# Kernel optimization log

Hardware: AMD Instinct MI355X
Metric: run time of the kernel (lower is better)

Reference implementation:

```python
import jax, jax.numpy as jnp
import numpy as np

N, E, FIN, H, OUT, L = 80000, 1280000, 128, 64, 10, 3
NEG_SLOPE = 0.2


def setup_inputs() -> dict:
    key = jax.random.key(0)
    ks = jax.random.split(key, 2 + 6 * L + 2)
    inp = {
        "x": jax.random.normal(ks[0], (N, FIN), dtype=jnp.float32),
        "edge_index": jax.random.randint(ks[1], (2, E), 0, N, dtype=jnp.int32),
        "batch": jnp.zeros((N,), dtype=jnp.int32),
    }
    k = 2
    for l in range(L):
        fin = FIN if l == 0 else H
        s = 1.0 / np.sqrt(fin)
        inp[f"Wl{l}"] = jax.random.normal(ks[k + 0], (H, fin), dtype=jnp.float32) * s
        inp[f"bl{l}"] = jnp.zeros((H,), dtype=jnp.float32)
        inp[f"Wr{l}"] = jax.random.normal(ks[k + 1], (H, fin), dtype=jnp.float32) * s
        inp[f"br{l}"] = jnp.zeros((H,), dtype=jnp.float32)
        inp[f"att{l}"] = jax.random.normal(ks[k + 2], (H,), dtype=jnp.float32) * (1.0 / np.sqrt(H))
        inp[f"b{l}"] = jnp.zeros((H,), dtype=jnp.float32)
        k += 3
    inp["Wro"] = jax.random.normal(ks[k], (OUT, H), dtype=jnp.float32) * (1.0 / np.sqrt(H))
    inp["bro"] = jnp.zeros((OUT,), dtype=jnp.float32)
    return inp


def gatv2_layer(h, src, dst, Wl, bl, Wr, br, att, b):
    # PyG GATv2Conv (heads=1, share_weights=False):
    #   xl = lin_l(h) (source side), xr = lin_r(h) (target side)
    xl = h @ Wl.T + bl          # [N, H]
    xr = h @ Wr.T + br          # [N, H]
    e = jax.nn.leaky_relu(xl[src] + xr[dst], NEG_SLOPE) @ att  # [E_tot]
    # softmax over incoming edges of each destination node
    m = jax.ops.segment_max(e, dst, num_segments=N)
    ex = jnp.exp(e - m[dst])
    denom = jax.ops.segment_sum(ex, dst, num_segments=N)
    alpha = ex / denom[dst]
    out = jax.ops.segment_sum(alpha[:, None] * xl[src], dst, num_segments=N)
    return out + b


def reference(x, edge_index, batch,
              Wl0, bl0, Wr0, br0, att0, b0,
              Wl1, bl1, Wr1, br1, att1, b1,
              Wl2, bl2, Wr2, br2, att2, b2,
              Wro, bro):
    # add self-loops once (same augmented edge set used each layer)
    loop = jnp.arange(N, dtype=edge_index.dtype)
    src = jnp.concatenate([edge_index[0], loop])
    dst = jnp.concatenate([edge_index[1], loop])
    layers = [
        (Wl0, bl0, Wr0, br0, att0, b0),
        (Wl1, bl1, Wr1, br1, att1, b1),
        (Wl2, bl2, Wr2, br2, att2, b2),
    ]
    h = x
    for (Wl, bl, Wr, br, att, b) in layers:
        h = jax.nn.relu(gatv2_layer(h, src, dst, Wl, bl, Wr, br, att, b))
    # graph_level_task=False: node-level readout
    return h @ Wro.T + bro  # [N, OUT]
```

## Files before the change

### kernel.cpp

```cpp
#include <hip/hip_runtime.h>
#include <hip/hip_bf16.h>
#include <hip/hip_fp16.h>


#define NN 80000
#define EE 1280000
#define FIN 128
#define HH 64
#define OUTD 10
#define NBUK 79
#define PCH 2048
#define NCH 625

typedef __hip_bfloat16 bf16;
typedef _Float16 f16x8 __attribute__((ext_vector_type(8)));
typedef float f32x4 __attribute__((ext_vector_type(4)));

__device__ __forceinline__ float ldw(const void* p, int i, int f) {
    return f ? __bfloat162float(((const bf16*)p)[i]) : ((const float*)p)[i];
}

__global__ void detect_kernel(const unsigned* __restrict__ w, int* __restrict__ flag) {
    int lane = threadIdx.x;
    int big = 0;
    for (int i = lane; i < 2048; i += 64) {
        unsigned u = w[i];
        float a = __uint_as_float(u << 16);
        float b = __uint_as_float(u & 0xffff0000u);
        if (!(fabsf(a) <= 1024.f)) big = 1;
        if (!(fabsf(b) <= 1024.f)) big = 1;
    }
    big = (__ballot(big) != 0ull) ? 1 : 0;
    if (lane == 0) flag[0] = big ? 0 : 1;
}

__global__ void preconvert(
    const void* Wl0, const void* Wr0, const void* Wl1, const void* Wr1,
    const void* Wl2, const void* Wr2,
    const void* bl0, const void* br0, const void* bl1, const void* br1,
    const void* bl2, const void* br2,
    const void* att0, const void* att1, const void* att2,
    const void* b0, const void* b1, const void* b2,
    const void* Wro, const void* bro,
    __half* Wh0, __half* Wh1, __half* Wh2, float* small,
    const int* __restrict__ flagp)
{
    const int f = flagp[0];
    int t = blockIdx.x * 256 + threadIdx.x;
    if (t < 16384) {
        int j = t & 127, k = t >> 7;
        float v = (j < 64) ? ldw(Wl0, j * 128 + k, f) : ldw(Wr0, (j - 64) * 128 + k, f);
        Wh0[j * 128 + k] = __float2half(v);
    } else if (t < 24576) {
        int u = t - 16384; int j = u & 127, k = u >> 7;
        float v = (j < 64) ? ldw(Wl1, j * 64 + k, f) : ldw(Wr1, (j - 64) * 64 + k, f);
        Wh1[j * 64 + k] = __float2half(v);
    } else if (t < 32768) {
        int u = t - 24576; int j = u & 127, k = u >> 7;
        float v = (j < 64) ? ldw(Wl2, j * 64 + k, f) : ldw(Wr2, (j - 64) * 64 + k, f);
        Wh2[j * 64 + k] = __float2half(v);
    } else if (t < 34304) {
        int s = t - 32768;
        const void* BL[3] = { bl0, bl1, bl2 };
        const void* BR[3] = { br0, br1, br2 };
        const void* AT[3] = { att0, att1, att2 };
        const void* BB[3] = { b0, b1, b2 };
        float v = 0.f;
        if (s < 384) {
            int l = s / 128, r = s % 128;
            v = (r < 64) ? ldw(BL[l], r, f) : ldw(BR[l], r - 64, f);
        } else if (s < 576) {
            int q = s - 384; v = ldw(AT[q / 64], q % 64, f);
        } else if (s < 768) {
            int q = s - 576; v = ldw(BB[q / 64], q % 64, f);
        } else if (s < 1408) {
            v = ldw(Wro, s - 768, f);
        } else if (s < 1418) {
            v = ldw(bro, s - 1408, f);
        } else return;
        small[s] = v;
    }
}

__global__ __launch_bounds__(256) void chunkhist_kernel(const int* __restrict__ dst,
                                                        int* __restrict__ chunkcnt)
{
    __shared__ int h[NBUK];
    const int tid = threadIdx.x, c = blockIdx.x;
    for (int i = tid; i < NBUK; i += 256) h[i] = 0;
    __syncthreads();
    const int e0 = c * PCH + tid * 8;
    int4 a = *(const int4*)(dst + e0);
    int4 b = *(const int4*)(dst + e0 + 4);
    atomicAdd(&h[a.x >> 10], 1); atomicAdd(&h[a.y >> 10], 1);
    atomicAdd(&h[a.z >> 10], 1); atomicAdd(&h[a.w >> 10], 1);
    atomicAdd(&h[b.x >> 10], 1); atomicAdd(&h[b.y >> 10], 1);
    atomicAdd(&h[b.z >> 10], 1); atomicAdd(&h[b.w >> 10], 1);
    __syncthreads();
    for (int i = tid; i < NBUK; i += 256) chunkcnt[i * NCH + c] = h[i];
}

__global__ __launch_bounds__(1024) void cscan_kernel(int* __restrict__ chunkcnt,
                                                     int* __restrict__ bucket_cnt)
{
    __shared__ int s[1024];
    const int b = blockIdx.x, t = threadIdx.x;
    int v = (t < NCH) ? chunkcnt[b * NCH + t] : 0;
    s[t] = v;
    __syncthreads();
    #pragma unroll
    for (int off = 1; off < 1024; off <<= 1) {
        int u = (t >= off) ? s[t - off] : 0;
        __syncthreads();
        s[t] += u;
        __syncthreads();
    }
    if (t < NCH) chunkcnt[b * NCH + t] = s[t] - v;
    if (t == NCH - 1) bucket_cnt[b] = s[t];
}

__global__ void bscan_kernel(const int* __restrict__ bucket_cnt,
                             int* __restrict__ bucket_base)
{
    __shared__ int sc[128];
    const int t = threadIdx.x;
    sc[t] = (t < NBUK) ? bucket_cnt[t] : 0;
    __syncthreads();
    #pragma unroll
    for (int off = 1; off < 128; off <<= 1) {
        int v = (t >= off) ? sc[t - off] : 0;
        __syncthreads();
        sc[t] += v;
        __syncthreads();
    }
    if (t < NBUK) bucket_base[t] = (t == 0) ? 0 : sc[t - 1];
    if (t == 0) bucket_base[NBUK] = sc[NBUK - 1];
}

__global__ __launch_bounds__(256) void part_kernel(const int* __restrict__ src,
                                                   const int* __restrict__ dst,
                                                   const int* __restrict__ chunkcnt,
                                                   const int* __restrict__ bucket_base,
                                                   int2* __restrict__ part)
{
    __shared__ int hcnt[NBUK];
    __shared__ int sc[128];
    __shared__ int hbase[NBUK + 1];
    __shared__ int hpos[NBUK];
    __shared__ int hgb[NBUK];
    __shared__ int2 stage[PCH];
    const int tid = threadIdx.x, c = blockIdx.x;

    for (int i = tid; i < NBUK; i += 256) hcnt[i] = 0;
    __syncthreads();

    const int e0 = c * PCH + tid * 8;
    int4 sa = *(const int4*)(src + e0);
    int4 sb = *(const int4*)(src + e0 + 4);
    int4 da = *(const int4*)(dst + e0);
    int4 db = *(const int4*)(dst + e0 + 4);
    int dv[8] = { da.x, da.y, da.z, da.w, db.x, db.y, db.z, db.w };
    int sv[8] = { sa.x, sa.y, sa.z, sa.w, sb.x, sb.y, sb.z, sb.w };
    #pragma unroll
    for (int u = 0; u < 8; u++) atomicAdd(&hcnt[dv[u] >> 10], 1);
    __syncthreads();

    if (tid < 128) sc[tid] = (tid < NBUK) ? hcnt[tid] : 0;
    __syncthreads();
    #pragma unroll
    for (int off = 1; off < 128; off <<= 1) {
        int v = (tid < 128 && tid >= off) ? sc[tid - off] : 0;
        __syncthreads();
        if (tid < 128) sc[tid] += v;
        __syncthreads();
    }
    if (tid < NBUK) {
        int b = (tid == 0) ? 0 : sc[tid - 1];
        hbase[tid] = b;
        hpos[tid] = b;
        hgb[tid] = bucket_base[tid] + chunkcnt[tid * NCH + c];
    }
    if (tid == 0) hbase[NBUK] = PCH;
    __syncthreads();

    #pragma unroll
    for (int u = 0; u < 8; u++) {
        int p = atomicAdd(&hpos[dv[u] >> 10], 1);
        stage[p] = make_int2(sv[u], dv[u]);
    }
    __syncthreads();

    for (int s = tid; s < PCH; s += 256) {
        int lo = 0, hi = NBUK;
        #pragma unroll
        for (int it = 0; it < 7; it++) {
            int mid = (lo + hi) >> 1;
            if (hbase[mid] <= s) lo = mid; else hi = mid;
        }
        part[hgb[lo] + (s - hbase[lo])] = stage[s];
    }
}

__global__ __launch_bounds__(256) void hist_part_kernel(const int2* __restrict__ part,
                                                        const int* __restrict__ bucket_base,
                                                        int* __restrict__ cnt)
{
    __shared__ int lcnt[1024];
    const int b = blockIdx.x, tid = threadIdx.x;
    const int dbase = b << 10;
    for (int i = tid; i < 1024; i += 256) lcnt[i] = 0;
    __syncthreads();
    const int eb = bucket_base[b], ee = bucket_base[b + 1];
    for (int e = eb + tid; e < ee; e += 256)
        atomicAdd(&lcnt[part[e].y - dbase], 1);
    __syncthreads();
    const int nd = min(1024, NN - dbase);
    for (int i = tid; i < nd; i += 256) cnt[dbase + i] = lcnt[i];
}

__global__ void scan1(const int* __restrict__ cnt, int* __restrict__ rowptr,
                      int* __restrict__ bsums) {
    __shared__ int sh[256];
    int i = blockIdx.x * 256 + threadIdx.x;
    int tid = threadIdx.x;
    int c = (i < NN) ? cnt[i] : 0;
    sh[tid] = c;
    __syncthreads();
    #pragma unroll
    for (int off = 1; off < 256; off <<= 1) {
        int t = (tid >= off) ? sh[tid - off] : 0;
        __syncthreads();
        sh[tid] += t;
        __syncthreads();
    }
    if (i < NN) rowptr[i + 1] = sh[tid];
    if (tid == 255) bsums[blockIdx.x] = sh[255];
}

__global__ void scan2(int* __restrict__ bsums, int nb) {
    __shared__ int sh[512];
    int t = threadIdx.x;
    sh[t] = (t < nb) ? bsums[t] : 0;
    __syncthreads();
    #pragma unroll
    for (int off = 1; off < 512; off <<= 1) {
        int v = (t >= off) ? sh[t - off] : 0;
        __syncthreads();
        sh[t] += v;
        __syncthreads();
    }
    if (t < nb) bsums[t] = sh[t];
}

__global__ void scan3(int* __restrict__ rowptr, const int* __restrict__ bsums) {
    int i = blockIdx.x * 256 + threadIdx.x;
    if (i == 0) rowptr[0] = 0;
    int add = (blockIdx.x == 0) ? 0 : bsums[blockIdx.x - 1];
    if (i < NN) rowptr[i + 1] += add;
}

__global__ __launch_bounds__(256) void scatter2_kernel(const int2* __restrict__ part,
                                                       const int* __restrict__ bucket_base,
                                                       const int* __restrict__ rowptr,
                                                       int2* __restrict__ col2)
{
    __shared__ int lfill[1024];
    const int b = blockIdx.x, tid = threadIdx.x;
    const int dbase = b << 10;
    const int nd = min(1024, NN - dbase);
    for (int i = tid; i < nd; i += 256) lfill[i] = rowptr[dbase + i];
    __syncthreads();
    const int eb = bucket_base[b], ee = bucket_base[b + 1];
    for (int e = eb + tid; e < ee; e += 256) {
        int2 sd = part[e];
        int pos = atomicAdd(&lfill[sd.y - dbase], 1);
        col2[pos] = sd;
    }
}

#define ELX_S 72
#define EXR_S 68
template<int F, bool L0>
__global__ __launch_bounds__(256) void lin_mfma(const void* __restrict__ hin_,
                                                const __half* __restrict__ Wh,
                                                const float* __restrict__ biasLR,
                                                __half* __restrict__ xlh,
                                                float* __restrict__ xr,
                                                const int* __restrict__ flagp)
{
    __shared__ __align__(16) char lds[64 * ELX_S * 2 + 64 * EXR_S * 4];
    _Float16* xs  = (_Float16*)lds;
    _Float16* eXL = (_Float16*)lds;
    float*    eXR = (float*)(lds + 64 * ELX_S * 2);

    const int tid = threadIdx.x;
    const int nb = blockIdx.x * 64;
    constexpr int OPR = F / 8;

    if (L0 && flagp[0]) {
        const uint4* hp = (const uint4*)hin_;
        for (int c = tid; c < 64 * OPR; c += 256) {
            int row = c / OPR, oct = c % OPR;
            uint4 u = hp[((size_t)(nb + row) * F + oct * 8) >> 3];
            unsigned ww[4] = { u.x, u.y, u.z, u.w };
            _Float16 v[8];
            #pragma unroll
            for (int p = 0; p < 4; p++) {
                v[2 * p]     = (_Float16)__uint_as_float(ww[p] << 16);
                v[2 * p + 1] = (_Float16)__uint_as_float(ww[p] & 0xffff0000u);
            }
            int so = oct ^ (row & 7);
            *(f16x8*)&xs[row * F + so * 8] = *(f16x8*)v;
        }
    } else {
        const float4* hp = (const float4*)hin_;
        for (int c = tid; c < 64 * OPR; c += 256) {
            int row = c / OPR, oct = c % OPR;
            size_t base = ((size_t)(nb + row) * F + oct * 8) >> 2;
            float4 a = hp[base], b = hp[base + 1];
            _Float16 v[8] = { (_Float16)a.x, (_Float16)a.y, (_Float16)a.z, (_Float16)a.w,
                              (_Float16)b.x, (_Float16)b.y, (_Float16)b.z, (_Float16)b.w };
            int so = oct ^ (row & 7);
            *(f16x8*)&xs[row * F + so * 8] = *(f16x8*)v;
        }
    }
    __syncthreads();

    const int w = tid >> 6;
    const int lane = tid & 63;
    const int n = lane & 15;
    const int quad = lane >> 4;
    constexpr int NS = F / 32;

    f16x8 afr[NS];
    #pragma unroll
    for (int s = 0; s < NS; s++) {
        int o = (s * 4 + quad) ^ (n & 7);
        afr[s] = *(const f16x8*)&xs[(w * 16 + n) * F + o * 8];
    }
    __syncthreads();

    const _Float16* Whf = (const _Float16*)Wh;
    #pragma unroll
    for (int ct = 0; ct < 8; ct++) {
        float bv = biasLR[ct * 16 + n];
        f32x4 acc = { bv, bv, bv, bv };
        #pragma unroll
        for (int s = 0; s < NS; s++) {
            f16x8 bfr = *(const f16x8*)&Whf[(size_t)(ct * 16 + n) * F + s * 32 + quad * 8];
            acc = __builtin_amdgcn_mfma_f32_16x16x32_f16(afr[s], bfr, acc, 0, 0, 0);
        }
        int rbase = w * 16 + quad * 4;
        if (ct < 4) {
            #pragma unroll
            for (int rg = 0; rg < 4; rg++)
                eXL[(rbase + rg) * ELX_S + ct * 16 + n] = (_Float16)acc[rg];
        } else {
            #pragma unroll
            for (int rg = 0; rg < 4; rg++)
                eXR[(rbase + rg) * EXR_S + (ct - 4) * 16 + n] = acc[rg];
        }
    }
    __syncthreads();

    for (int c = tid; c < 512; c += 256) {
        int row = c >> 3, oct = c & 7;
        *(uint4*)&xlh[(size_t)(nb + row) * 64 + oct * 8] =
            *(const uint4*)&eXL[row * ELX_S + oct * 8];
    }
    for (int c = tid; c < 1024; c += 256) {
        int row = c >> 4, q4 = c & 15;
        *(float4*)&xr[(size_t)(nb + row) * 64 + q4 * 4] =
            *(const float4*)&eXR[row * EXR_S + q4 * 4];
    }
}

#define DECODE8(U, D) { \
    float2 _f0 = __half22float2(*(__half2*)&U.x); \
    float2 _f1 = __half22float2(*(__half2*)&U.y); \
    float2 _f2 = __half22float2(*(__half2*)&U.z); \
    float2 _f3 = __half22float2(*(__half2*)&U.w); \
    D[0]=_f0.x; D[1]=_f0.y; D[2]=_f1.x; D[3]=_f1.y; \
    D[4]=_f2.x; D[5]=_f2.y; D[6]=_f3.x; D[7]=_f3.y; }

__global__ __launch_bounds__(256) void agg4_kernel(const __half* __restrict__ xlh,
                                                   const float* __restrict__ xr,
                                                   const float* __restrict__ attf,
                                                   const float* __restrict__ bf,
                                                   const int* __restrict__ rowptr,
                                                   const int2* __restrict__ col2,
                                                   float* __restrict__ hout)
{
    const int lane = threadIdx.x & 63;
    const int g = lane >> 3;
    const int r = lane & 7;
    int iw = blockIdx.x * 4 + (threadIdx.x >> 6);
    if (iw >= NN) return;
    const int i = __builtin_amdgcn_readfirstlane(iw);

    float xri[8], att[8];
    {
        float4 xa = *(const float4*)(xr + (size_t)i * 64 + r * 8);
        float4 xb = *(const float4*)(xr + (size_t)i * 64 + r * 8 + 4);
        xri[0]=xa.x; xri[1]=xa.y; xri[2]=xa.z; xri[3]=xa.w;
        xri[4]=xb.x; xri[5]=xb.y; xri[6]=xb.z; xri[7]=xb.w;
        float4 aa = *(const float4*)(attf + r * 8);
        float4 ab = *(const float4*)(attf + r * 8 + 4);
        att[0]=aa.x; att[1]=aa.y; att[2]=aa.z; att[3]=aa.w;
        att[4]=ab.x; att[5]=ab.y; att[6]=ab.z; att[7]=ab.w;
    }

    uint4 srow = *(const uint4*)(xlh + (size_t)i * 64 + r * 8);
    float s[8]; DECODE8(srow, s);
    float ps = 0.f;
    #pragma unroll
    for (int k = 0; k < 8; k++) {
        float u = s[k] + xri[k];
        ps = fmaf(att[k], fmaf(0.4f, fabsf(u), 0.6f * u), ps);
    }
    ps += __shfl_xor(ps, 1, 64);
    ps += __shfl_xor(ps, 2, 64);
    ps += __shfl_xor(ps, 4, 64);
    float wself = __expf(fminf(ps, 60.f));

    float acc[8];
    float denom;
    if (g == 0) {
        #pragma unroll
        for (int k = 0; k < 8; k++) acc[k] = wself * s[k];
        denom = wself;
    } else {
        #pragma unroll
        for (int k = 0; k < 8; k++) acc[k] = 0.f;
        denom = 0.f;
    }

    const int e0 = rowptr[i], e1 = rowptr[i + 1];
    const int n = e1 - e0;
    const int eL = e1 - 1;

    for (int base = 0; base < n; base += 16) {
        const int j = e0 + base;
        int sa = col2[min(j + g, eL)].x;
        int sb = col2[min(j + 8 + g, eL)].x;
        uint4 ua = *(const uint4*)(xlh + (size_t)sa * 64 + r * 8);
        uint4 ub = *(const uint4*)(xlh + (size_t)sb * 64 + r * 8);
        float A[8], B[8];
        DECODE8(ua, A);
        DECODE8(ub, B);

        float pa = 0.f, pb = 0.f;
        #pragma unroll
        for (int k = 0; k < 8; k++) {
            float va = A[k] + xri[k];
            float vb = B[k] + xri[k];
            pa = fmaf(att[k], fmaf(0.4f, fabsf(va), 0.6f * va), pa);
            pb = fmaf(att[k], fmaf(0.4f, fabsf(vb), 0.6f * vb), pb);
        }
        pa += __shfl_xor(pa, 1, 64);  pb += __shfl_xor(pb, 1, 64);
        pa += __shfl_xor(pa, 2, 64);  pb += __shfl_xor(pb, 2, 64);
        pa += __shfl_xor(pa, 4, 64);  pb += __shfl_xor(pb, 4, 64);

        float wa = (base + g < n)     ? __expf(fminf(pa, 60.f)) : 0.f;
        float wb = (base + 8 + g < n) ? __expf(fminf(pb, 60.f)) : 0.f;

        #pragma unroll
        for (int k = 0; k < 8; k++) {
            acc[k] = fmaf(wa, A[k], acc[k]);
            acc[k] = fmaf(wb, B[k], acc[k]);
        }
        denom += wa + wb;
    }

    #pragma unroll
    for (int off = 8; off < 64; off <<= 1) {
        #pragma unroll
        for (int k = 0; k < 8; k++) acc[k] += __shfl_xor(acc[k], off, 64);
        denom += __shfl_xor(denom, off, 64);
    }

    if (g == 0) {
        float inv = 1.f / denom;
        float4 bfa = *(const float4*)(bf + r * 8);
        float4 bfb = *(const float4*)(bf + r * 8 + 4);
        float o0 = fmaxf(fmaf(acc[0], inv, bfa.x), 0.f);
        float o1 = fmaxf(fmaf(acc[1], inv, bfa.y), 0.f);
        float o2 = fmaxf(fmaf(acc[2], inv, bfa.z), 0.f);
        float o3 = fmaxf(fmaf(acc[3], inv, bfa.w), 0.f);
        float o4 = fmaxf(fmaf(acc[4], inv, bfb.x), 0.f);
        float o5 = fmaxf(fmaf(acc[5], inv, bfb.y), 0.f);
        float o6 = fmaxf(fmaf(acc[6], inv, bfb.z), 0.f);
        float o7 = fmaxf(fmaf(acc[7], inv, bfb.w), 0.f);
        float* op = hout + (size_t)i * 64 + r * 8;
        *(float4*)(op)     = make_float4(o0, o1, o2, o3);
        *(float4*)(op + 4) = make_float4(o4, o5, o6, o7);
    }
}

__global__ __launch_bounds__(256) void readout2_kernel(const float* __restrict__ h,
                                                       const float* __restrict__ WROf,
                                                       const float* __restrict__ brof,
                                                       void* __restrict__ out,
                                                       const int* __restrict__ flagp)
{
    __shared__ float wsh[640];
    __shared__ float bsh[OUTD];
    const int tid = threadIdx.x;
    for (int idx = tid; idx < 640; idx += 256) {
        int k = idx / 10, o = idx % 10;
        wsh[idx] = WROf[o * 64 + k];
    }
    if (tid < OUTD) bsh[tid] = brof[tid];
    __syncthreads();

    const int i = blockIdx.x * 256 + tid;
    if (i >= NN) return;
    const int f = flagp[0];

    float res[OUTD];
    #pragma unroll
    for (int o = 0; o < OUTD; o++) res[o] = bsh[o];

    const float4* h4 = (const float4*)(h + (size_t)i * 64);
    #pragma unroll 4
    for (int c = 0; c < 16; c++) {
        float4 hv = h4[c];
        const float* wp = &wsh[c * 40];
        #pragma unroll
        for (int o = 0; o < OUTD; o++) {
            float t = fmaf(hv.x, wp[o], fmaf(hv.y, wp[10 + o],
                      fmaf(hv.z, wp[20 + o], hv.w * wp[30 + o])));
            res[o] += t;
        }
    }

    if (f) {
        bf16* op = (bf16*)out + (size_t)i * OUTD;
        #pragma unroll
        for (int o = 0; o < OUTD; o++) op[o] = __float2bfloat16(res[o]);
    } else {
        float* op = (float*)out + (size_t)i * OUTD;
        #pragma unroll
        for (int o = 0; o < OUTD; o++) op[o] = res[o];
    }
}

extern "C" void kernel_launch(void* const* d_in, const int* in_sizes, int n_in,
                              void* d_out, int out_size, void* d_ws, size_t ws_size,
                              hipStream_t stream) {
    const void* x   = d_in[0];
    const int* ei   = (const int*)d_in[1];
    const void* Wl0 = d_in[3];  const void* bl0 = d_in[4];
    const void* Wr0 = d_in[5];  const void* br0 = d_in[6];
    const void* at0 = d_in[7];  const void* b0  = d_in[8];
    const void* Wl1 = d_in[9];  const void* bl1 = d_in[10];
    const void* Wr1 = d_in[11]; const void* br1 = d_in[12];
    const void* at1 = d_in[13]; const void* b1  = d_in[14];
    const void* Wl2 = d_in[15]; const void* bl2 = d_in[16];
    const void* Wr2 = d_in[17]; const void* br2 = d_in[18];
    const void* at2 = d_in[19]; const void* b2  = d_in[20];
    const void* Wro = d_in[21]; const void* bro = d_in[22];

    const int* srcArr = ei;
    const int* dstArr = ei + EE;

    float* wf = (float*)d_ws;
    __half* Wh0  = (__half*)wf;
    __half* Wh1  = (__half*)(wf + 16384);
    __half* Wh2  = (__half*)(wf + 24576);
    float* small = wf + 32768;
    int*   flag  = (int*)(wf + 34304);
    int*   rowptr = (int*)(wf + 34368);
    int*   bsums  = (int*)(wf + 114496);
    int*   fillc  = (int*)(wf + 115008);
    int*   bucket_cnt  = (int*)(wf + 195008);
    int*   bucket_base = (int*)(wf + 195136);
    int*   chunkcnt    = (int*)(wf + 195264);
    int2*  part   = (int2*)(wf + 244736);
    int2*  col2   = (int2*)(wf + 2804736);
    __half* xlh   = (__half*)(wf + 5364736);
    float* xr = wf + 7924736;
    float* hA = xr + (size_t)NN * 64;

    float* biasLR0 = small;        float* biasLR1 = small + 128; float* biasLR2 = small + 256;
    float* attf0 = small + 384;    float* attf1 = small + 448;   float* attf2 = small + 512;
    float* bf0   = small + 576;    float* bf1   = small + 640;   float* bf2   = small + 704;
    float* WROf  = small + 768;    float* brof  = small + 1408;

    detect_kernel<<<dim3(1), dim3(64), 0, stream>>>((const unsigned*)Wl0, flag);

    preconvert<<<dim3(134), dim3(256), 0, stream>>>(
        Wl0, Wr0, Wl1, Wr1, Wl2, Wr2, bl0, br0, bl1, br1, bl2, br2,
        at0, at1, at2, b0, b1, b2, Wro, bro, Wh0, Wh1, Wh2, small, flag);

    chunkhist_kernel<<<dim3(NCH), dim3(256), 0, stream>>>(dstArr, chunkcnt);
    cscan_kernel<<<dim3(NBUK), dim3(1024), 0, stream>>>(chunkcnt, bucket_cnt);
    bscan_kernel<<<dim3(1), dim3(128), 0, stream>>>(bucket_cnt, bucket_base);
    part_kernel<<<dim3(NCH), dim3(256), 0, stream>>>(srcArr, dstArr, chunkcnt, bucket_base, part);
    hist_part_kernel<<<dim3(NBUK), dim3(256), 0, stream>>>(part, bucket_base, fillc);
    scan1<<<dim3(313), dim3(256), 0, stream>>>(fillc, rowptr, bsums);
    scan2<<<dim3(1), dim3(512), 0, stream>>>(bsums, 313);
    scan3<<<dim3(313), dim3(256), 0, stream>>>(rowptr, bsums);
    scatter2_kernel<<<dim3(NBUK), dim3(256), 0, stream>>>(part, bucket_base, rowptr, col2);

    lin_mfma<128, true><<<dim3(NN / 64), dim3(256), 0, stream>>>(x, Wh0, biasLR0, xlh, xr, flag);
    agg4_kernel<<<dim3(NN / 4), dim3(256), 0, stream>>>(xlh, xr, attf0, bf0, rowptr, col2, hA);
    lin_mfma<64, false><<<dim3(NN / 64), dim3(256), 0, stream>>>(hA, Wh1, biasLR1, xlh, xr, flag);
    agg4_kernel<<<dim3(NN / 4), dim3(256), 0, stream>>>(xlh, xr, attf1, bf1, rowptr, col2, hA);
    lin_mfma<64, false><<<dim3(NN / 64), dim3(256), 0, stream>>>(hA, Wh2, biasLR2, xlh, xr, flag);
    agg4_kernel<<<dim3(NN / 4), dim3(256), 0, stream>>>(xlh, xr, attf2, bf2, rowptr, col2, hA);

    readout2_kernel<<<dim3(313), dim3(256), 0, stream>>>(hA, WROf, brof, d_out, flag);
}
```

Measured before the change: 414.4 us.

## Split leaky-ReLU into linear and abs parts with per-node precomputed att dots

Rewrites leaky_relu(u) as 0.6u + 0.4|u|, so the linear part att·xl[src] + att·xr[dst] is computed once per node in the linear kernel (slp/srp) and only the abs term stays per edge. The CSR column array shrinks from int2 to int, halving index traffic, and the edge loop is split into a full-16 main loop with no bounds checks plus a remainder path. In exchange, each edge does an extra scalar gather of slp[src], and the epilogue of the linear kernel does a little more work.

```diff
diff --git a/kernel.cpp b/kernel.cpp
--- a/kernel.cpp
+++ b/kernel.cpp
@@ -262,7 +262,7 @@
 __global__ __launch_bounds__(256) void scatter2_kernel(const int2* __restrict__ part,
                                                        const int* __restrict__ bucket_base,
                                                        const int* __restrict__ rowptr,
-                                                       int2* __restrict__ col2)
+                                                       int* __restrict__ col)
 {
     __shared__ int lfill[1024];
     const int b = blockIdx.x, tid = threadIdx.x;
@@ -274,7 +274,7 @@
     for (int e = eb + tid; e < ee; e += 256) {
         int2 sd = part[e];
         int pos = atomicAdd(&lfill[sd.y - dbase], 1);
-        col2[pos] = sd;
+        col[pos] = sd.x;
     }
 }
 
@@ -284,8 +284,11 @@
 __global__ __launch_bounds__(256) void lin_mfma(const void* __restrict__ hin_,
                                                 const __half* __restrict__ Wh,
                                                 const float* __restrict__ biasLR,
+                                                const float* __restrict__ attf,
                                                 __half* __restrict__ xlh,
                                                 float* __restrict__ xr,
+                                                float* __restrict__ slp,
+                                                float* __restrict__ srp,
                                                 const int* __restrict__ flagp)
 {
     __shared__ __align__(16) char lds[64 * ELX_S * 2 + 64 * EXR_S * 4];
@@ -373,6 +376,36 @@
         *(float4*)&xr[(size_t)(nb + row) * 64 + q4 * 4] =
             *(const float4*)&eXR[row * EXR_S + q4 * 4];
     }
+
+    if (tid < 64) {
+        float accl = 0.f, accr = 0.f;
+        #pragma unroll
+        for (int o = 0; o < 8; o++) {
+            f16x8 vl = *(const f16x8*)&eXL[tid * ELX_S + o * 8];
+            float4 a0 = *(const float4*)(attf + o * 8);
+            float4 a1 = *(const float4*)(attf + o * 8 + 4);
+            float4 v0 = *(const float4*)&eXR[tid * EXR_S + o * 8];
+            float4 v1 = *(const float4*)&eXR[tid * EXR_S + o * 8 + 4];
+            accl = fmaf(a0.x, (float)vl[0], accl);
+            accl = fmaf(a0.y, (float)vl[1], accl);
+            accl = fmaf(a0.z, (float)vl[2], accl);
+            accl = fmaf(a0.w, (float)vl[3], accl);
+            accl = fmaf(a1.x, (float)vl[4], accl);
+            accl = fmaf(a1.y, (float)vl[5], accl);
+            accl = fmaf(a1.z, (float)vl[6], accl);
+            accl = fmaf(a1.w, (float)vl[7], accl);
+            accr = fmaf(a0.x, v0.x, accr);
+            accr = fmaf(a0.y, v0.y, accr);
+            accr = fmaf(a0.z, v0.z, accr);
+            accr = fmaf(a0.w, v0.w, accr);
+            accr = fmaf(a1.x, v1.x, accr);
+            accr = fmaf(a1.y, v1.y, accr);
+            accr = fmaf(a1.z, v1.z, accr);
+            accr = fmaf(a1.w, v1.w, accr);
+        }
+        slp[nb + tid] = accl;
+        srp[nb + tid] = accr;
+    }
 }
 
 #define DECODE8(U, D) { \
@@ -383,12 +416,14 @@
     D[0]=_f0.x; D[1]=_f0.y; D[2]=_f1.x; D[3]=_f1.y; \
     D[4]=_f2.x; D[5]=_f2.y; D[6]=_f3.x; D[7]=_f3.y; }
 
-__global__ __launch_bounds__(256) void agg4_kernel(const __half* __restrict__ xlh,
+__global__ __launch_bounds__(256) void agg5_kernel(const __half* __restrict__ xlh,
                                                    const float* __restrict__ xr,
+                                                   const float* __restrict__ slp,
+                                                   const float* __restrict__ srp,
                                                    const float* __restrict__ attf,
                                                    const float* __restrict__ bf,
                                                    const int* __restrict__ rowptr,
-                                                   const int2* __restrict__ col2,
+                                                   const int* __restrict__ col,
                                                    float* __restrict__ hout)
 {
     const int lane = threadIdx.x & 63;
@@ -409,19 +444,19 @@
         att[0]=aa.x; att[1]=aa.y; att[2]=aa.z; att[3]=aa.w;
         att[4]=ab.x; att[5]=ab.y; att[6]=ab.z; att[7]=ab.w;
     }
+    const float sri06 = 0.6f * srp[i];
 
     uint4 srow = *(const uint4*)(xlh + (size_t)i * 64 + r * 8);
     float s[8]; DECODE8(srow, s);
     float ps = 0.f;
     #pragma unroll
-    for (int k = 0; k < 8; k++) {
-        float u = s[k] + xri[k];
-        ps = fmaf(att[k], fmaf(0.4f, fabsf(u), 0.6f * u), ps);
-    }
+    for (int k = 0; k < 8; k++)
+        ps = fmaf(att[k], fabsf(s[k] + xri[k]), ps);
     ps += __shfl_xor(ps, 1, 64);
     ps += __shfl_xor(ps, 2, 64);
     ps += __shfl_xor(ps, 4, 64);
-    float wself = __expf(fminf(ps, 60.f));
+    float es = fmaf(0.4f, ps, fmaf(0.6f, slp[i], sri06));
+    float wself = __expf(fminf(es, 60.f));
 
     float acc[8];
     float denom;
@@ -437,12 +472,14 @@
 
     const int e0 = rowptr[i], e1 = rowptr[i + 1];
     const int n = e1 - e0;
-    const int eL = e1 - 1;
-
-    for (int base = 0; base < n; base += 16) {
+    const int nfull = n & ~15;
+
+    int base = 0;
+    for (; base < nfull; base += 16) {
         const int j = e0 + base;
-        int sa = col2[min(j + g, eL)].x;
-        int sb = col2[min(j + 8 + g, eL)].x;
+        int sa = col[j + g];
+        int sb = col[j + 8 + g];
+        float sla = slp[sa], slb = slp[sb];
         uint4 ua = *(const uint4*)(xlh + (size_t)sa * 64 + r * 8);
         uint4 ub = *(const uint4*)(xlh + (size_t)sb * 64 + r * 8);
         float A[8], B[8];
@@ -452,17 +489,17 @@
         float pa = 0.f, pb = 0.f;
         #pragma unroll
         for (int k = 0; k < 8; k++) {
-            float va = A[k] + xri[k];
-            float vb = B[k] + xri[k];
-            pa = fmaf(att[k], fmaf(0.4f, fabsf(va), 0.6f * va), pa);
-            pb = fmaf(att[k], fmaf(0.4f, fabsf(vb), 0.6f * vb), pb);
+            pa = fmaf(att[k], fabsf(A[k] + xri[k]), pa);
+            pb = fmaf(att[k], fabsf(B[k] + xri[k]), pb);
         }
         pa += __shfl_xor(pa, 1, 64);  pb += __shfl_xor(pb, 1, 64);
         pa += __shfl_xor(pa, 2, 64);  pb += __shfl_xor(pb, 2, 64);
         pa += __shfl_xor(pa, 4, 64);  pb += __shfl_xor(pb, 4, 64);
 
-        float wa = (base + g < n)     ? __expf(fminf(pa, 60.f)) : 0.f;
-        float wb = (base + 8 + g < n) ? __expf(fminf(pb, 60.f)) : 0.f;
+        float ea = fmaf(0.4f, pa, fmaf(0.6f, sla, sri06));
+        float eb = fmaf(0.4f, pb, fmaf(0.6f, slb, sri06));
+        float wa = __expf(fminf(ea, 60.f));
+        float wb = __expf(fminf(eb, 60.f));
 
         #pragma unroll
         for (int k = 0; k < 8; k++) {
@@ -470,6 +507,66 @@
             acc[k] = fmaf(wb, B[k], acc[k]);
         }
         denom += wa + wb;
+    }
+
+    const int rem = n - base;
+    if (rem > 0) {
+        const int j = e0 + base;
+        const int eL = e1 - 1;
+        if (rem > 8) {
+            int sa = col[j + g];
+            int sb = col[min(j + 8 + g, eL)];
+            float sla = slp[sa], slb = slp[sb];
+            uint4 ua = *(const uint4*)(xlh + (size_t)sa * 64 + r * 8);
+            uint4 ub = *(const uint4*)(xlh + (size_t)sb * 64 + r * 8);
+            float A[8], B[8];
+            DECODE8(ua, A);
+            DECODE8(ub, B);
+
+            float pa = 0.f, pb = 0.f;
+            #pragma unroll
+            for (int k = 0; k < 8; k++) {
+                pa = fmaf(att[k], fabsf(A[k] + xri[k]), pa);
+                pb = fmaf(att[k], fabsf(B[k] + xri[k]), pb);
+            }
+            pa += __shfl_xor(pa, 1, 64);  pb += __shfl_xor(pb, 1, 64);
+            pa += __shfl_xor(pa, 2, 64);  pb += __shfl_xor(pb, 2, 64);
+            pa += __shfl_xor(pa, 4, 64);  pb += __shfl_xor(pb, 4, 64);
+
+            float ea = fmaf(0.4f, pa, fmaf(0.6f, sla, sri06));
+            float eb = fmaf(0.4f, pb, fmaf(0.6f, slb, sri06));
+            float wa = __expf(fminf(ea, 60.f));
+            float wb = (8 + g < rem) ? __expf(fminf(eb, 60.f)) : 0.f;
+
+            #pragma unroll
+            for (int k = 0; k < 8; k++) {
+                acc[k] = fmaf(wa, A[k], acc[k]);
+                acc[k] = fmaf(wb, B[k], acc[k]);
+            }
+            denom += wa + wb;
+        } else {
+            int sa = col[min(j + g, eL)];
+            float sla = slp[sa];
+            uint4 ua = *(const uint4*)(xlh + (size_t)sa * 64 + r * 8);
+            float A[8];
+            DECODE8(ua, A);
+
+            float pa = 0.f;
+            #pragma unroll
+            for (int k = 0; k < 8; k++)
+                pa = fmaf(att[k], fabsf(A[k] + xri[k]), pa);
+            pa += __shfl_xor(pa, 1, 64);
+            pa += __shfl_xor(pa, 2, 64);
+            pa += __shfl_xor(pa, 4, 64);
+
+            float ea = fmaf(0.4f, pa, fmaf(0.6f, sla, sri06));
+            float wa = (g < rem) ? __expf(fminf(ea, 60.f)) : 0.f;
+
+            #pragma unroll
+            for (int k = 0; k < 8; k++)
+                acc[k] = fmaf(wa, A[k], acc[k]);
+            denom += wa;
+        }
     }
 
     #pragma unroll
@@ -577,7 +674,9 @@
     int*   bucket_base = (int*)(wf + 195136);
     int*   chunkcnt    = (int*)(wf + 195264);
     int2*  part   = (int2*)(wf + 244736);
-    int2*  col2   = (int2*)(wf + 2804736);
+    int*   col    = (int*)(wf + 2804736);
+    float* slp    = wf + 4084736;
+    float* srp    = wf + 4164736;
     __half* xlh   = (__half*)(wf + 5364736);
     float* xr = wf + 7924736;
     float* hA = xr + (size_t)NN * 64;
@@ -601,14 +700,14 @@
     scan1<<<dim3(313), dim3(256), 0, stream>>>(fillc, rowptr, bsums);
     scan2<<<dim3(1), dim3(512), 0, stream>>>(bsums, 313);
     scan3<<<dim3(313), dim3(256), 0, stream>>>(rowptr, bsums);
-    scatter2_kernel<<<dim3(NBUK), dim3(256), 0, stream>>>(part, bucket_base, rowptr, col2);
-
-    lin_mfma<128, true><<<dim3(NN / 64), dim3(256), 0, stream>>>(x, Wh0, biasLR0, xlh, xr, flag);
-    agg4_kernel<<<dim3(NN / 4), dim3(256), 0, stream>>>(xlh, xr, attf0, bf0, rowptr, col2, hA);
-    lin_mfma<64, false><<<dim3(NN / 64), dim3(256), 0, stream>>>(hA, Wh1, biasLR1, xlh, xr, flag);
-    agg4_kernel<<<dim3(NN / 4), dim3(256), 0, stream>>>(xlh, xr, attf1, bf1, rowptr, col2, hA);
-    lin_mfma<64, false><<<dim3(NN / 64), dim3(256), 0, stream>>>(hA, Wh2, biasLR2, xlh, xr, flag);
-    agg4_kernel<<<dim3(NN / 4), dim3(256), 0, stream>>>(xlh, xr, attf2, bf2, rowptr, col2, hA);
+    scatter2_kernel<<<dim3(NBUK), dim3(256), 0, stream>>>(part, bucket_base, rowptr, col);
+
+    lin_mfma<128, true><<<dim3(NN / 64), dim3(256), 0, stream>>>(x, Wh0, biasLR0, attf0, xlh, xr, slp, srp, flag);
+    agg5_kernel<<<dim3(NN / 4), dim3(256), 0, stream>>>(xlh, xr, slp, srp, attf0, bf0, rowptr, col, hA);
+    lin_mfma<64, false><<<dim3(NN / 64), dim3(256), 0, stream>>>(hA, Wh1, biasLR1, attf1, xlh, xr, slp, srp, flag);
+    agg5_kernel<<<dim3(NN / 4), dim3(256), 0, stream>>>(xlh, xr, slp, srp, attf1, bf1, rowptr, col, hA);
+    lin_mfma<64, false><<<dim3(NN / 64), dim3(256), 0, stream>>>(hA, Wh2, biasLR2, attf2, xlh, xr, slp, srp, flag);
+    agg5_kernel<<<dim3(NN / 4), dim3(256), 0, stream>>>(xlh, xr, slp, srp, attf2, bf2, rowptr, col, hA);
 
     readout2_kernel<<<dim3(313), dim3(256), 0, stream>>>(hA, WROf, brof, d_out, flag);
 }
```

Result: faster. 402.2 us (-3.0%).
